# Optimization experiments

Measured on AMD Instinct MI355X. Metric: run time of the kernel, lower is better.

The kernel has to match this reference:

```python
import jax, jax.numpy as jnp
import numpy as np
import math

B, T, C = 4, 2048, 2048
NUM_HEADS = 16
HEAD_DIM = C // NUM_HEADS  # 128
ROPE_BASE = 10000.0


def _rope_tables(t, head_dim, dtype):
    # inv_freq over even dims; emb = concat(freqs, freqs)
    inv_freq = 1.0 / (ROPE_BASE ** (jnp.arange(0, head_dim, 2, dtype=jnp.float32) / head_dim))
    pos = jnp.arange(t, dtype=jnp.float32)
    freqs = jnp.einsum('i,j->ij', pos, inv_freq)          # [t, head_dim/2]
    emb = jnp.concatenate([freqs, freqs], axis=-1)        # [t, head_dim]
    return jnp.cos(emb).astype(dtype), jnp.sin(emb).astype(dtype)


def _rotate_half(x):
    x1, x2 = jnp.split(x, 2, axis=-1)
    return jnp.concatenate([-x2, x1], axis=-1)


def setup_inputs() -> dict:
    key = jax.random.key(0)
    ks = jax.random.split(key, 5)
    scale = 1.0 / math.sqrt(C)
    x = jax.random.normal(ks[0], (B, T, C), dtype=jnp.float32)
    wq = jax.random.normal(ks[1], (C, C), dtype=jnp.float32) * scale
    wk = jax.random.normal(ks[2], (C, C), dtype=jnp.float32) * scale
    wv = jax.random.normal(ks[3], (C, C), dtype=jnp.float32) * scale
    wo = jax.random.normal(ks[4], (C, C), dtype=jnp.float32) * scale
    mask = jnp.tril(jnp.ones((T, T), dtype=jnp.int32))[None, None]  # causal [1,1,T,T]
    return {"x": x, "mask": mask, "wq": wq, "wk": wk, "wv": wv, "wo": wo}


def reference(x, mask, wq, wk, wv, wo):
    b, t, c = x.shape
    h, hd = NUM_HEADS, HEAD_DIM
    # torch Linear: y = x @ W.T (W is [out,in])
    q = (x @ wq.T).reshape(b, t, h, hd).transpose(0, 2, 1, 3)  # [b,h,t,hd]
    k = (x @ wk.T).reshape(b, t, h, hd).transpose(0, 2, 1, 3)
    v = (x @ wv.T).reshape(b, t, h, hd).transpose(0, 2, 1, 3)
    cos, sin = _rope_tables(t, hd, x.dtype)  # [t,hd] each, broadcast over b,h
    q = q * cos + _rotate_half(q) * sin
    k = k * cos + _rotate_half(k) * sin
    att = jnp.einsum('bhqd,bhkd->bhqk', q, k) * (1.0 / math.sqrt(hd))
    att = jnp.where(mask == 0, -jnp.inf, att)
    att = jax.nn.softmax(att, axis=-1)
    y = jnp.einsum('bhqk,bhkd->bhqd', att, v)
    y = y.transpose(0, 2, 1, 3).reshape(b, t, c)
    return y @ wo.T
```

## Files before the change

kernel.cpp:

```cpp
#include <hip/hip_runtime.h>
#include <hip/hip_bf16.h>

#define BB 4
#define TT 2048
#define CC 2048
#define NH 16
#define HD 128
#define BT (BB*TT)

using u16 = unsigned short;
typedef __bf16 bf16x8 __attribute__((ext_vector_type(8)));
typedef float  f32x4  __attribute__((ext_vector_type(4)));

#define AS1 __attribute__((address_space(1)))
#define AS3 __attribute__((address_space(3)))

__device__ __forceinline__ float b2f(u16 u){ return __uint_as_float(((unsigned)u) << 16); }
__device__ __forceinline__ u16 f2b(float f){
  unsigned u = __float_as_uint(f);
  u += 0x7FFFu + ((u >> 16) & 1u);
  return (u16)(u >> 16);
}
__device__ __forceinline__ void gld_lds16(const u16* g, u16* l){
  __builtin_amdgcn_global_load_lds((const AS1 void*)g, (AS3 void*)l, 16, 0, 0);
}

__global__ __launch_bounds__(256) void cvt_kernel(const float* __restrict__ in,
                                                  u16* __restrict__ out, int n8)
{
  const int i = blockIdx.x * 256 + threadIdx.x;
  if (i >= n8) return;
  const float4 a = ((const float4*)in)[2*i];
  const float4 b = ((const float4*)in)[2*i + 1];
  uint4 pk;
  pk.x = (unsigned)f2b(a.x) | ((unsigned)f2b(a.y) << 16);
  pk.y = (unsigned)f2b(a.z) | ((unsigned)f2b(a.w) << 16);
  pk.z = (unsigned)f2b(b.x) | ((unsigned)f2b(b.y) << 16);
  pk.w = (unsigned)f2b(b.z) | ((unsigned)f2b(b.w) << 16);
  ((uint4*)out)[i] = pk;
}

template<bool OUT_BF16>
__global__ __launch_bounds__(512, 2) void gemm256(const u16* __restrict__ A,
                                                  const u16* __restrict__ W,
                                                  void* __restrict__ Cv,
                                                  int K, int N)
{
  __shared__ u16 lds[65536];
  const int tid  = threadIdx.x;
  const int lane = tid & 63;
  const int wid  = tid >> 6;
  const int wm   = wid >> 2;
  const int wn   = wid & 3;

  const int nwg  = (int)(gridDim.x * gridDim.y);
  const int orig = (int)(blockIdx.y * gridDim.x + blockIdx.x);
  const int swz  = (orig & 7) * (nwg >> 3) + (orig >> 3);
  const int bx   = swz % (int)gridDim.x;
  const int by   = swz / (int)gridDim.x;
  const long mbase = (long)by * 256;
  const long nbase = (long)bx * 256;

  const int sR  = tid >> 2;
  const int sG8 = (((tid & 3) ^ (sR & 3)) << 3);
  const u16* gA = A + (mbase + sR) * (long)K + sG8;
  const u16* gB = W + (nbase + sR) * (long)K + sG8;
  const long rowK = (long)128 * K;

  const int n   = lane & 15;
  const int g   = lane >> 4;
  const int sl8 = ((g ^ (n & 3)) << 3);
  const int aoff = (wm*128 + n)*32 + sl8;
  const int boff = 8192 + (wn*64 + n)*32 + sl8;

  f32x4 acc[8][4] = {};
  const int NT = K >> 5;

#define STAGE_A(bufi, tt) do { \
    u16* d_ = lds + (bufi)*16384 + tid*8; \
    gld_lds16(gA + (long)(tt)*32,        d_); \
    gld_lds16(gA + rowK + (long)(tt)*32, d_ + 4096); } while(0)
#define STAGE_B(bufi, tt) do { \
    u16* d_ = lds + (bufi)*16384 + 8192 + tid*8; \
    gld_lds16(gB + (long)(tt)*32,        d_); \
    gld_lds16(gB + rowK + (long)(tt)*32, d_ + 4096); } while(0)

  STAGE_A(0, 0); STAGE_B(0, 0);
  STAGE_A(1, 1); STAGE_B(1, 1);
  asm volatile("s_waitcnt vmcnt(4)" ::: "memory");
  __builtin_amdgcn_s_barrier();

  for (int t = 0; t < NT; ++t) {
    const u16* Ab = lds + (t & 3) * 16384;
    bf16x8 a0[4], b0[4], a1[4];
    #pragma unroll
    for (int i = 0; i < 4; i++) a0[i] = *(const bf16x8*)&Ab[aoff + i*512];
    #pragma unroll
    for (int j = 0; j < 4; j++) b0[j] = *(const bf16x8*)&Ab[boff + j*512];
    if (t + 2 < NT) STAGE_A((t+2)&3, t+2);
    __builtin_amdgcn_s_barrier();
    __builtin_amdgcn_s_setprio(1);
    #pragma unroll
    for (int i = 0; i < 4; i++)
      #pragma unroll
      for (int j = 0; j < 4; j++)
        acc[i][j] = __builtin_amdgcn_mfma_f32_16x16x32_bf16(a0[i], b0[j], acc[i][j], 0,0,0);
    __builtin_amdgcn_s_setprio(0);
    __builtin_amdgcn_s_barrier();
    #pragma unroll
    for (int i = 0; i < 4; i++) a1[i] = *(const bf16x8*)&Ab[aoff + (i+4)*512];
    if (t + 2 < NT) STAGE_B((t+2)&3, t+2);
    __builtin_amdgcn_s_barrier();
    __builtin_amdgcn_s_setprio(1);
    #pragma unroll
    for (int i = 0; i < 4; i++)
      #pragma unroll
      for (int j = 0; j < 4; j++)
        acc[i+4][j] = __builtin_amdgcn_mfma_f32_16x16x32_bf16(a1[i], b0[j], acc[i+4][j], 0,0,0);
    __builtin_amdgcn_s_setprio(0);
    if (t + 2 < NT) { asm volatile("s_waitcnt vmcnt(4)" ::: "memory"); }
    else            { asm volatile("s_waitcnt vmcnt(0)" ::: "memory"); }
    __builtin_amdgcn_s_barrier();
  }
#undef STAGE_A
#undef STAGE_B

  const int crow0 = g * 4;
  #pragma unroll
  for (int i = 0; i < 8; i++)
    #pragma unroll
    for (int j = 0; j < 4; j++)
      #pragma unroll
      for (int r = 0; r < 4; r++) {
        const long row = mbase + wm*128 + i*16 + crow0 + r;
        const long col = nbase + wn*64  + j*16 + n;
        if (OUT_BF16) ((u16*)Cv)[row*N + col]   = f2b(acc[i][j][r]);
        else          ((float*)Cv)[row*N + col] = acc[i][j][r];
      }
}

__global__ __launch_bounds__(256) void rope_kernel(u16* __restrict__ q, u16* __restrict__ k)
{
  const unsigned idx = blockIdx.x * 256u + threadIdx.x;
  const int d = idx & 63;
  const int h = (idx >> 6) & 15;
  const int t = (idx >> 10) & 2047;
  const int b = idx >> 21;
  const float inv = __expf(-9.210340371976184f * ((float)d * (1.0f/64.0f)));
  const float ang = (float)t * inv;
  float sn, cs;
  sincosf(ang, &sn, &cs);
  const size_t base = ((size_t)(b * TT + t)) * CC + (size_t)h * HD + d;
  const float q0 = b2f(q[base]), q1 = b2f(q[base + 64]);
  q[base]      = f2b(q0*cs - q1*sn);
  q[base + 64] = f2b(q1*cs + q0*sn);
  const float k0 = b2f(k[base]), k1 = b2f(k[base + 64]);
  k[base]      = f2b(k0*cs - k1*sn);
  k[base + 64] = f2b(k1*cs + k0*sn);
}

__global__ __launch_bounds__(256) void transpose_v(const u16* __restrict__ v,
                                                   u16* __restrict__ vt)
{
  __shared__ u16 L[64][136];
  const int tid = threadIdx.x;
  const int t0 = blockIdx.x * 64;
  const int b = blockIdx.y >> 4, h = blockIdx.y & 15;
  #pragma unroll
  for (int it = 0; it < 4; it++) {
    const int row = (tid >> 4) + it*16;
    const int c8 = (tid & 15) * 8;
    *(uint4*)&L[row][c8] = *(const uint4*)(v + ((size_t)(b*TT + t0 + row))*CC + h*HD + c8);
  }
  __syncthreads();
  #pragma unroll
  for (int it = 0; it < 4; it++) {
    const int hd = (tid >> 3) + it*32;
    const int c = (tid & 7) * 8;
    u16 tmp[8];
    #pragma unroll
    for (int j = 0; j < 8; j++) tmp[j] = L[c + j][hd];
    uint4 pk;
    pk.x = (unsigned)tmp[0] | ((unsigned)tmp[1] << 16);
    pk.y = (unsigned)tmp[2] | ((unsigned)tmp[3] << 16);
    pk.z = (unsigned)tmp[4] | ((unsigned)tmp[5] << 16);
    pk.w = (unsigned)tmp[6] | ((unsigned)tmp[7] << 16);
    *(uint4*)(vt + ((size_t)((b*NH + h)*HD + hd))*TT + t0 + c) = pk;
  }
}

#define KS_ST 136
#define VS_ST 72
#define PS_ST 72
__global__ __launch_bounds__(256, 2) void attn_mfma(const u16* __restrict__ q,
                                                    const u16* __restrict__ k,
                                                    const u16* __restrict__ vt,
                                                    u16* __restrict__ y)
{
  __shared__ u16 smem[64*KS_ST + 128*VS_ST + 4*32*PS_ST];
  u16* Ks = smem;
  u16* Vs = smem + 64*KS_ST;
  u16* Ps = smem + 64*KS_ST + 128*VS_ST;

  const int tid  = threadIdx.x;
  const int lane = tid & 63;
  const int w    = tid >> 6;
  const int n    = lane & 15;
  const int g    = lane >> 4;
  const int k8   = g * 8;
  const int qb   = (int)gridDim.x - 1 - (int)blockIdx.x;
  const int bh   = blockIdx.y;
  const int b = bh >> 4, h = bh & 15;

  const u16* Qg  = q  + (size_t)b*TT*CC + (size_t)h*HD;
  const u16* Kg  = k  + (size_t)b*TT*CC + (size_t)h*HD;
  const u16* Vtg = vt + ((size_t)(b*NH + h)*HD) * TT;
  u16*       Yg  = y  + (size_t)b*TT*CC + (size_t)h*HD;

  bf16x8 qf[2][4];
  #pragma unroll
  for (int mi = 0; mi < 2; mi++)
    #pragma unroll
    for (int s = 0; s < 4; s++)
      qf[mi][s] = *(const bf16x8*)(Qg + (size_t)(qb*128 + w*32 + mi*16 + n)*CC + s*32 + k8);

  f32x4 o[8][2] = {};
  float lrow[2][4] = {};

  u16* Psw = Ps + w * 32 * PS_ST;
  const float scale = 0.08838834764831845f;
  const int ktmax = 2*qb + 1;

  for (int kt = 0; kt <= ktmax; kt++) {
    __syncthreads();
    #pragma unroll
    for (int it = 0; it < 4; it++) {
      const int row = (tid >> 4) + it*16;
      const int c8 = (tid & 15) * 8;
      *(uint4*)&Ks[row*KS_ST + c8] = *(const uint4*)(Kg + (size_t)(kt*64 + row)*CC + c8);
    }
    #pragma unroll
    for (int it = 0; it < 4; it++) {
      const int row = (tid >> 3) + it*32;
      const int c8 = (tid & 7) * 8;
      *(uint4*)&Vs[row*VS_ST + c8] = *(const uint4*)(Vtg + (size_t)row*TT + kt*64 + c8);
    }
    __syncthreads();

    f32x4 sacc[4][2] = {};
    #pragma unroll
    for (int s = 0; s < 4; s++) {
      #pragma unroll
      for (int j = 0; j < 4; j++) {
        const bf16x8 kb = *(const bf16x8*)&Ks[(16*j + n)*KS_ST + 32*s + k8];
        sacc[j][0] = __builtin_amdgcn_mfma_f32_16x16x32_bf16(qf[0][s], kb, sacc[j][0], 0,0,0);
        sacc[j][1] = __builtin_amdgcn_mfma_f32_16x16x32_bf16(qf[1][s], kb, sacc[j][1], 0,0,0);
      }
    }

    if (kt >= 2*qb) {
      #pragma unroll
      for (int mi = 0; mi < 2; mi++)
        #pragma unroll
        for (int j = 0; j < 4; j++)
          #pragma unroll
          for (int r = 0; r < 4; r++) {
            const int kcol = kt*64 + 16*j + n;
            const int qrow = qb*128 + w*32 + mi*16 + 4*g + r;
            if (kcol > qrow) sacc[j][mi][r] = -1e30f;
          }
    }

    #pragma unroll
    for (int mi = 0; mi < 2; mi++)
      #pragma unroll
      for (int j = 0; j < 4; j++)
        #pragma unroll
        for (int r = 0; r < 4; r++) {
          const float p = __expf(sacc[j][mi][r] * scale);
          lrow[mi][r] += p;
          Psw[(mi*16 + 4*g + r)*PS_ST + 16*j + n] = f2b(p);
        }

    __syncthreads();

    #pragma unroll
    for (int s2 = 0; s2 < 2; s2++) {
      const bf16x8 pa0 = *(const bf16x8*)&Psw[(n)*PS_ST      + s2*32 + k8];
      const bf16x8 pa1 = *(const bf16x8*)&Psw[(16 + n)*PS_ST + s2*32 + k8];
      #pragma unroll
      for (int jo = 0; jo < 8; jo++) {
        const bf16x8 vb = *(const bf16x8*)&Vs[(16*jo + n)*VS_ST + s2*32 + k8];
        o[jo][0] = __builtin_amdgcn_mfma_f32_16x16x32_bf16(pa0, vb, o[jo][0], 0,0,0);
        o[jo][1] = __builtin_amdgcn_mfma_f32_16x16x32_bf16(pa1, vb, o[jo][1], 0,0,0);
      }
    }
  }

  #pragma unroll
  for (int mi = 0; mi < 2; mi++)
    #pragma unroll
    for (int r = 0; r < 4; r++) {
      float sv = lrow[mi][r];
      #pragma unroll
      for (int msk = 1; msk <= 8; msk <<= 1) sv += __shfl_xor(sv, msk);
      lrow[mi][r] = sv;
    }

  __syncthreads();
  u16* Ob = smem;
  #pragma unroll
  for (int mi = 0; mi < 2; mi++) {
    float inv[4];
    #pragma unroll
    for (int r = 0; r < 4; r++) inv[r] = 1.0f / lrow[mi][r];
    #pragma unroll
    for (int jo = 0; jo < 8; jo++)
      #pragma unroll
      for (int r = 0; r < 4; r++)
        Ob[(w*32 + mi*16 + 4*g + r)*KS_ST + 16*jo + n] = f2b(o[jo][mi][r] * inv[r]);
  }
  __syncthreads();
  #pragma unroll
  for (int it = 0; it < 8; it++) {
    const int idx = it*64 + lane;
    const int row = idx >> 4;
    const int ch  = (idx & 15) * 8;
    const uint4 pk = *(const uint4*)&Ob[(w*32 + row)*KS_ST + ch];
    *(uint4*)(Yg + (size_t)(qb*128 + w*32 + row)*CC + ch) = pk;
  }
}

extern "C" void kernel_launch(void* const* d_in, const int* in_sizes, int n_in,
                              void* d_out, int out_size, void* d_ws, size_t ws_size,
                              hipStream_t stream)
{
  const float* x  = (const float*)d_in[0];
  const float* wq = (const float*)d_in[2];
  const float* wk = (const float*)d_in[3];
  const float* wv = (const float*)d_in[4];
  const float* wo = (const float*)d_in[5];

  const size_t NE  = (size_t)BT * CC;
  const size_t NW  = (size_t)CC * CC;
  u16* q  = (u16*)d_ws;
  u16* k  = q  + NE;
  u16* v  = k  + NE;
  u16* y  = v  + NE;
  u16* xb = y  + NE;
  u16* wqb = xb + NE;
  u16* wkb = wqb + NW;
  u16* wvb = wkb + NW;
  u16* wob = wvb + NW;
  u16* vt  = xb;

  cvt_kernel<<<(int)(NE/8/256), 256, 0, stream>>>(x,  xb,  (int)(NE/8));
  cvt_kernel<<<(int)(NW/8/256), 256, 0, stream>>>(wq, wqb, (int)(NW/8));
  cvt_kernel<<<(int)(NW/8/256), 256, 0, stream>>>(wk, wkb, (int)(NW/8));
  cvt_kernel<<<(int)(NW/8/256), 256, 0, stream>>>(wv, wvb, (int)(NW/8));
  cvt_kernel<<<(int)(NW/8/256), 256, 0, stream>>>(wo, wob, (int)(NW/8));

  const dim3 gg(CC/256, BT/256);
  gemm256<true><<<gg, 512, 0, stream>>>(xb, wqb, q, CC, CC);
  gemm256<true><<<gg, 512, 0, stream>>>(xb, wkb, k, CC, CC);
  gemm256<true><<<gg, 512, 0, stream>>>(xb, wvb, v, CC, CC);

  rope_kernel<<<(BB*TT*NH*64)/256, 256, 0, stream>>>(q, k);

  transpose_v<<<dim3(TT/64, BB*NH), 256, 0, stream>>>(v, vt);

  attn_mfma<<<dim3(TT/128, BB*NH), 256, 0, stream>>>(q, k, vt, y);

  gemm256<false><<<gg, 512, 0, stream>>>(y, wob, (float*)d_out, CC, CC);
}
```

Baseline: 661.9 us.

## Deepen GEMM LDS prefetch to three stages and register-prefetch K/V in attention

The GEMM main loop now keeps three tiles in flight in its 4-buffer LDS ring instead of two, with vmcnt waits adjusted for the tail iterations. The attention kernel loads the next K/V tile into registers while the current tile is being computed, writes it to LDS after the PV MFMAs, and raises wave priority around the MFMA blocks. Both changes aim to hide global memory latency behind matrix math. The cost is more registers for the prefetch buffers and a deeper dependency on the buffer-reuse ordering, which may lower occupancy.

New measurement: 877.9 us. 1.33x slower.

```diff
diff --git a/kernel.cpp b/kernel.cpp
--- a/kernel.cpp
+++ b/kernel.cpp
@@ -87,7 +87,8 @@
 
   STAGE_A(0, 0); STAGE_B(0, 0);
   STAGE_A(1, 1); STAGE_B(1, 1);
-  asm volatile("s_waitcnt vmcnt(4)" ::: "memory");
+  STAGE_A(2, 2); STAGE_B(2, 2);
+  asm volatile("s_waitcnt vmcnt(8)" ::: "memory");
   __builtin_amdgcn_s_barrier();
 
   for (int t = 0; t < NT; ++t) {
@@ -97,7 +98,7 @@
     for (int i = 0; i < 4; i++) a0[i] = *(const bf16x8*)&Ab[aoff + i*512];
     #pragma unroll
     for (int j = 0; j < 4; j++) b0[j] = *(const bf16x8*)&Ab[boff + j*512];
-    if (t + 2 < NT) STAGE_A((t+2)&3, t+2);
+    if (t + 3 < NT) STAGE_A((t+3)&3, t+3);
     __builtin_amdgcn_s_barrier();
     __builtin_amdgcn_s_setprio(1);
     #pragma unroll
@@ -109,7 +110,7 @@
     __builtin_amdgcn_s_barrier();
     #pragma unroll
     for (int i = 0; i < 4; i++) a1[i] = *(const bf16x8*)&Ab[aoff + (i+4)*512];
-    if (t + 2 < NT) STAGE_B((t+2)&3, t+2);
+    if (t + 3 < NT) STAGE_B((t+3)&3, t+3);
     __builtin_amdgcn_s_barrier();
     __builtin_amdgcn_s_setprio(1);
     #pragma unroll
@@ -118,8 +119,9 @@
       for (int j = 0; j < 4; j++)
         acc[i+4][j] = __builtin_amdgcn_mfma_f32_16x16x32_bf16(a1[i], b0[j], acc[i+4][j], 0,0,0);
     __builtin_amdgcn_s_setprio(0);
-    if (t + 2 < NT) { asm volatile("s_waitcnt vmcnt(4)" ::: "memory"); }
-    else            { asm volatile("s_waitcnt vmcnt(0)" ::: "memory"); }
+    if (t + 3 < NT)      { asm volatile("s_waitcnt vmcnt(8)" ::: "memory"); }
+    else if (t + 2 < NT) { asm volatile("s_waitcnt vmcnt(4)" ::: "memory"); }
+    else                 { asm volatile("s_waitcnt vmcnt(0)" ::: "memory"); }
     __builtin_amdgcn_s_barrier();
   }
 #undef STAGE_A
@@ -217,6 +219,11 @@
   const u16* Vtg = vt + ((size_t)(b*NH + h)*HD) * TT;
   u16*       Yg  = y  + (size_t)b*TT*CC + (size_t)h*HD;
 
+  const int krow = tid >> 4;
+  const int kc8  = (tid & 15) * 8;
+  const int vrow = tid >> 3;
+  const int vc8  = (tid & 7) * 8;
+
   bf16x8 qf[2][4];
   #pragma unroll
   for (int mi = 0; mi < 2; mi++)
@@ -231,23 +238,37 @@
   const float scale = 0.08838834764831845f;
   const int ktmax = 2*qb + 1;
 
+  {
+    uint4 kp[4], vp[4];
+    #pragma unroll
+    for (int it = 0; it < 4; it++)
+      kp[it] = *(const uint4*)(Kg + (size_t)(krow + it*16)*CC + kc8);
+    #pragma unroll
+    for (int it = 0; it < 4; it++)
+      vp[it] = *(const uint4*)(Vtg + (size_t)(vrow + it*32)*TT + vc8);
+    #pragma unroll
+    for (int it = 0; it < 4; it++)
+      *(uint4*)&Ks[(krow + it*16)*KS_ST + kc8] = kp[it];
+    #pragma unroll
+    for (int it = 0; it < 4; it++)
+      *(uint4*)&Vs[(vrow + it*32)*VS_ST + vc8] = vp[it];
+  }
+  __syncthreads();
+
   for (int kt = 0; kt <= ktmax; kt++) {
-    __syncthreads();
-    #pragma unroll
-    for (int it = 0; it < 4; it++) {
-      const int row = (tid >> 4) + it*16;
-      const int c8 = (tid & 15) * 8;
-      *(uint4*)&Ks[row*KS_ST + c8] = *(const uint4*)(Kg + (size_t)(kt*64 + row)*CC + c8);
-    }
-    #pragma unroll
-    for (int it = 0; it < 4; it++) {
-      const int row = (tid >> 3) + it*32;
-      const int c8 = (tid & 7) * 8;
-      *(uint4*)&Vs[row*VS_ST + c8] = *(const uint4*)(Vtg + (size_t)row*TT + kt*64 + c8);
-    }
-    __syncthreads();
+    uint4 kp[4], vp[4];
+    const bool pf = (kt < ktmax);
+    if (pf) {
+      #pragma unroll
+      for (int it = 0; it < 4; it++)
+        kp[it] = *(const uint4*)(Kg + (size_t)((kt+1)*64 + krow + it*16)*CC + kc8);
+      #pragma unroll
+      for (int it = 0; it < 4; it++)
+        vp[it] = *(const uint4*)(Vtg + (size_t)(vrow + it*32)*TT + (kt+1)*64 + vc8);
+    }
 
     f32x4 sacc[4][2] = {};
+    __builtin_amdgcn_s_setprio(1);
     #pragma unroll
     for (int s = 0; s < 4; s++) {
       #pragma unroll
@@ -257,6 +278,7 @@
         sacc[j][1] = __builtin_amdgcn_mfma_f32_16x16x32_bf16(qf[1][s], kb, sacc[j][1], 0,0,0);
       }
     }
+    __builtin_amdgcn_s_setprio(0);
 
     if (kt >= 2*qb) {
       #pragma unroll
@@ -284,6 +306,7 @@
 
     __syncthreads();
 
+    __builtin_amdgcn_s_setprio(1);
     #pragma unroll
     for (int s2 = 0; s2 < 2; s2++) {
       const bf16x8 pa0 = *(const bf16x8*)&Psw[(n)*PS_ST      + s2*32 + k8];
@@ -294,6 +317,18 @@
         o[jo][0] = __builtin_amdgcn_mfma_f32_16x16x32_bf16(pa0, vb, o[jo][0], 0,0,0);
         o[jo][1] = __builtin_amdgcn_mfma_f32_16x16x32_bf16(pa1, vb, o[jo][1], 0,0,0);
       }
+    }
+    __builtin_amdgcn_s_setprio(0);
+
+    __syncthreads();
+    if (pf) {
+      #pragma unroll
+      for (int it = 0; it < 4; it++)
+        *(uint4*)&Ks[(krow + it*16)*KS_ST + kc8] = kp[it];
+      #pragma unroll
+      for (int it = 0; it < 4; it++)
+        *(uint4*)&Vs[(vrow + it*32)*VS_ST + vc8] = vp[it];
+      __syncthreads();
     }
   }
 
```
